# Performance work log

Hardware: AMD Instinct MI355X
Metric: run time of the kernel (lower is better)

## Reference

```python
import jax, jax.numpy as jnp
import numpy as np
import math

B, N, DIM = 2, 4096, 1024
H, D, M = 16, 64, 256


def setup_inputs() -> dict:
    key = jax.random.key(0)
    ks = jax.random.split(key, 6)
    s = 1.0 / math.sqrt(DIM)
    return {
        "x": jax.random.normal(ks[0], (B, N, DIM), dtype=jnp.float32),
        "w_q": jax.random.normal(ks[1], (DIM, H * D), dtype=jnp.float32) * s,
        "w_k": jax.random.normal(ks[2], (DIM, H * D), dtype=jnp.float32) * s,
        "w_v": jax.random.normal(ks[3], (DIM, H * D), dtype=jnp.float32) * s,
        "w_o": jax.random.normal(ks[4], (H * D, DIM), dtype=jnp.float32) * s,
        "b_o": jnp.zeros((DIM,), dtype=jnp.float32),
        "omega": jax.random.normal(ks[5], (M, D), dtype=jnp.float32),
    }


def _heads(t):
    # [B, N, H*D] -> [B, H, N, D]
    return t.reshape(B, N, H, D).transpose(0, 2, 1, 3)


def _phi(t, omega):
    # t: [B,H,N,D], omega: [M,D] -> [B,H,N,M]
    proj = jnp.einsum("bhnd,md->bhnm", t, omega)
    norm = 0.5 * jnp.sum(t * t, axis=-1, keepdims=True)
    return jnp.exp(proj - norm) / math.sqrt(M)


def reference(x, w_q, w_k, w_v, w_o, b_o, omega):
    q = _heads(x @ w_q)
    k = _heads(x @ w_k)
    v = _heads(x @ w_v)
    phi_q = _phi(q, omega)          # [B,H,N,M]
    phi_k = _phi(k, omega)          # [B,H,N,M]
    kv = jnp.einsum("bhnm,bhnd->bhmd", phi_k, v)   # [B,H,M,D]
    k_sum = phi_k.sum(axis=2)                       # [B,H,M]
    z = 1.0 / (jnp.einsum("bhnm,bhm->bhn", phi_q, k_sum) + 1e-6)
    out = jnp.einsum("bhnm,bhmd->bhnd", phi_q, kv) * z[..., None]
    out = out.transpose(0, 2, 1, 3).reshape(B, N, H * D)
    return out @ w_o + b_o
```

## Files before the change

kernel.cpp:

```cpp
#include <hip/hip_runtime.h>

#define DEVI __device__ __forceinline__

using f32x4 = __attribute__((ext_vector_type(4))) float;
using fvec4 = __attribute__((ext_vector_type(4))) float;
using s16x4 = __attribute__((ext_vector_type(4))) short;
using s16x8 = __attribute__((ext_vector_type(8))) short;

DEVI unsigned short f2bf_rn(float f) {
  union { float f; unsigned u; } v; v.f = f;
  unsigned r = v.u + 0x7fffu + ((v.u >> 16) & 1u);
  return (unsigned short)(r >> 16);
}
DEVI float bf2f(unsigned short h) {
  union { unsigned u; float f; } v; v.u = ((unsigned)h) << 16;
  return v.f;
}
DEVI f32x4 mfma16(s16x8 a, s16x8 b, f32x4 c) {
  return __builtin_amdgcn_mfma_f32_16x16x32_bf16(a, b, c, 0, 0, 0);
}
DEVI void gld16(const void* g, void* lds) {
  __builtin_amdgcn_global_load_lds(
      (const __attribute__((address_space(1))) unsigned int*)g,
      (__attribute__((address_space(3))) unsigned int*)lds, 16, 0, 0);
}

__global__ __launch_bounds__(256) void k_prep_all(
    const float* __restrict__ wq, const float* __restrict__ wk,
    const float* __restrict__ wv, const float* __restrict__ wo,
    const float* __restrict__ omega, const float* __restrict__ X,
    unsigned short* __restrict__ WTh, unsigned short* __restrict__ WOT,
    unsigned short* __restrict__ OMB,
    unsigned short* __restrict__ XH, unsigned short* __restrict__ XL)
{
  __shared__ float tile[64][65];
  const int z = blockIdx.z;
  const int t = threadIdx.x;
  if (z >= 5) {
    int s = z - 5;
    int bid = blockIdx.x * 16 + blockIdx.y;
    size_t i = (((size_t)s * 256 + bid) * 256 + t) * 8;
    fvec4 a = *(const fvec4*)&X[i];
    fvec4 b = *(const fvec4*)&X[i + 4];
    s16x8 hv, lv;
#pragma unroll
    for (int j = 0; j < 4; ++j) {
      unsigned short h = f2bf_rn(a[j]);
      hv[j] = (short)h; lv[j] = (short)f2bf_rn(a[j] - bf2f(h));
    }
#pragma unroll
    for (int j = 0; j < 4; ++j) {
      unsigned short h = f2bf_rn(b[j]);
      hv[4 + j] = (short)h; lv[4 + j] = (short)f2bf_rn(b[j] - bf2f(h));
    }
    *(s16x8*)&XH[i] = hv;
    *(s16x8*)&XL[i] = lv;
    return;
  }
  if (z == 4) {
    int bid = blockIdx.x * 16 + blockIdx.y;
    if (bid < 16) {
      int i = (bid * 256 + t) * 4;
      fvec4 v = *(const fvec4*)&omega[i];
      s16x4 hv;
#pragma unroll
      for (int q = 0; q < 4; ++q) hv[q] = (short)f2bf_rn(v[q]);
      *(s16x4*)&OMB[i] = hv;
    }
    return;
  }
  const float* src = (z == 0) ? wq : (z == 1) ? wk : (z == 2) ? wv : wo;
  const int k0 = blockIdx.x * 64;
  const int n0 = blockIdx.y * 64;
#pragma unroll
  for (int j = 0; j < 4; ++j) {
    int r = (t >> 4) + 16 * j;
    int c = (t & 15) * 4;
    fvec4 v = *(const fvec4*)&src[(size_t)(k0 + r) * 1024 + n0 + c];
#pragma unroll
    for (int i = 0; i < 4; ++i) tile[r][c + i] = v[i];
  }
  __syncthreads();
#pragma unroll
  for (int j = 0; j < 4; ++j) {
    int n = (t >> 4) + 16 * j;
    int kc = (t & 15) * 4;
    s16x4 hv;
#pragma unroll
    for (int i = 0; i < 4; ++i) hv[i] = (short)f2bf_rn(tile[kc + i][n]);
    if (z < 3) {
      *(s16x4*)&WTh[(size_t)(z * 1024 + n0 + n) * 1024 + k0 + kc] = hv;
    } else {
      *(s16x4*)&WOT[(size_t)(n0 + n) * 1024 + k0 + kc] = hv;
    }
  }
}

__global__ __launch_bounds__(256) void k_gemm_qkv(
    const unsigned short* __restrict__ XH, const unsigned short* __restrict__ XL,
    const unsigned short* __restrict__ WTh,
    unsigned short* __restrict__ QH, unsigned short* __restrict__ QL,
    unsigned short* __restrict__ KH, unsigned short* __restrict__ KL,
    unsigned short* __restrict__ VB)
{
  __shared__ unsigned short AH[2][128 * 32];
  __shared__ unsigned short BHs[2][128 * 32];
  __shared__ unsigned short AL[2][128 * 32];
  const int flat = blockIdx.y * 24 + blockIdx.x;
  const int swz = (flat & 7) * 192 + (flat >> 3);
  const int cb = swz % 24;
  const int rb = swz / 24;
  const int t = threadIdx.x;
  const int w = t >> 6, l = t & 63;
  const bool tp = (cb < 16);
  f32x4 acc[4][4];
#pragma unroll
  for (int a = 0; a < 4; ++a)
#pragma unroll
    for (int b = 0; b < 4; ++b) acc[a][b] = (f32x4)0.f;

  const int r0 = w * 32;
  const int lrow = l >> 2;
  const int lcol = (l & 3) * 8;
  const size_t gA = (size_t)(rb * 128 + r0 + lrow) * 1024 + lcol;
  const size_t gB = (size_t)(cb * 128 + r0 + lrow) * 1024 + lcol;
  const int lds0 = r0 * 32;
  const int lds1 = (r0 + 16) * 32;

  const int wm = (w & 1) * 64, wn = (w >> 1) * 64;
  const int lr = l & 15, ko = (l >> 4) * 8;

  auto STAGE = [&](int buf, int k0) {
    gld16(&XH[gA + k0], &AH[buf][lds0]);
    gld16(&XH[gA + (size_t)16 * 1024 + k0], &AH[buf][lds1]);
    if (tp) {
      gld16(&XL[gA + k0], &AL[buf][lds0]);
      gld16(&XL[gA + (size_t)16 * 1024 + k0], &AL[buf][lds1]);
    }
    gld16(&WTh[gB + k0], &BHs[buf][lds0]);
    gld16(&WTh[gB + (size_t)16 * 1024 + k0], &BHs[buf][lds1]);
  };

  STAGE(0, 0);
  int cur = 0;
  for (int ks = 0; ks < 32; ++ks) {
    if (ks < 31) {
      STAGE(cur ^ 1, (ks + 1) * 32);
      if (tp) asm volatile("s_waitcnt vmcnt(6)" ::: "memory");
      else    asm volatile("s_waitcnt vmcnt(4)" ::: "memory");
    } else {
      asm volatile("s_waitcnt vmcnt(0)" ::: "memory");
    }
    __builtin_amdgcn_s_barrier();
    asm volatile("" ::: "memory");
    s16x8 ah[4], al[4], bh[4];
#pragma unroll
    for (int f = 0; f < 4; ++f) {
      ah[f] = *(const s16x8*)&AH[cur][(wm + f * 16 + lr) * 32 + ko];
      bh[f] = *(const s16x8*)&BHs[cur][(wn + f * 16 + lr) * 32 + ko];
    }
    if (tp) {
#pragma unroll
      for (int f = 0; f < 4; ++f) al[f] = *(const s16x8*)&AL[cur][(wm + f * 16 + lr) * 32 + ko];
    }
#pragma unroll
    for (int fa = 0; fa < 4; ++fa)
#pragma unroll
      for (int fb = 0; fb < 4; ++fb) {
        acc[fa][fb] = mfma16(ah[fa], bh[fb], acc[fa][fb]);
        if (tp) acc[fa][fb] = mfma16(al[fa], bh[fb], acc[fa][fb]);
      }
    asm volatile("s_waitcnt lgkmcnt(0)" ::: "memory");
    __builtin_amdgcn_s_barrier();
    asm volatile("" ::: "memory");
    cur ^= 1;
  }
  const int lg = l >> 4;
#pragma unroll
  for (int fa = 0; fa < 4; ++fa)
#pragma unroll
    for (int r = 0; r < 4; ++r) {
      int row = rb * 128 + wm + fa * 16 + lg * 4 + r;
#pragma unroll
      for (int fb = 0; fb < 4; ++fb) {
        int col = cb * 128 + wn + fb * 16 + lr;
        float v = acc[fa][fb][r];
        if (tp) {
          unsigned short hs = f2bf_rn(v);
          unsigned short ls = f2bf_rn(v - bf2f(hs));
          if (cb < 8) {
            QH[(size_t)row * 1024 + col] = hs;
            QL[(size_t)row * 1024 + col] = ls;
          } else {
            KH[(size_t)row * 1024 + col - 1024] = hs;
            KL[(size_t)row * 1024 + col - 1024] = ls;
          }
        } else {
          VB[(size_t)row * 1024 + col - 2048] = f2bf_rn(v);
        }
      }
    }
}

__global__ __launch_bounds__(512, 1) void k_phik_kv(
    const unsigned short* __restrict__ KH, const unsigned short* __restrict__ KL,
    const unsigned short* __restrict__ VB,
    const unsigned short* __restrict__ OMB, float* __restrict__ KVP)
{
  __shared__ unsigned short KHs[64][72], KLs[64][72];
  __shared__ unsigned short PKT[128][72];
  __shared__ unsigned short AVT[80][72];
  __shared__ float norm_s[64];
  const int nc = blockIdx.x;
  const int bh = blockIdx.y;
  const int mh = blockIdx.z;
  const int b = bh >> 4, h = bh & 15;
  const int t = threadIdx.x, w = t >> 6, l = t & 63;
  const int lr = l & 15, lg = l >> 4, ko8 = lg * 8;
  const int mg = mh * 128 + w * 16 + lr;

  s16x8 omf[2];
#pragma unroll
  for (int ksub = 0; ksub < 2; ++ksub)
    omf[ksub] = *(const s16x8*)&OMB[(size_t)mg * 64 + ksub * 32 + ko8];

  for (int e = t; e < 16 * 64; e += 512) {
    int rr = e >> 6, cc = e & 63;
    AVT[64 + rr][cc] = (rr == 0) ? (unsigned short)0x3F80 : (unsigned short)0;
  }

  f32x4 acc2[5];
#pragma unroll
  for (int a = 0; a < 5; ++a) acc2[a] = (f32x4)0.f;

  for (int st = 0; st < 8; ++st) {
    const int n0 = nc * 512 + st * 64;
    __syncthreads();
    {
      int r = t >> 3, c8 = (t & 7) * 8;
      size_t o = (size_t)(b * 4096 + n0 + r) * 1024 + h * 64 + c8;
      s16x8 vh = *(const s16x8*)&KH[o];
      s16x8 vl = *(const s16x8*)&KL[o];
      *(s16x8*)&KHs[r][c8] = vh;
      *(s16x8*)&KLs[r][c8] = vl;
      float ss = 0.f;
#pragma unroll
      for (int i = 0; i < 8; ++i) {
        float q = bf2f((unsigned short)vh[i]) + bf2f((unsigned short)vl[i]);
        ss += q * q;
      }
      ss += __shfl_xor(ss, 1);
      ss += __shfl_xor(ss, 2);
      ss += __shfl_xor(ss, 4);
      if ((t & 7) == 0) norm_s[r] = 0.5f * ss;
    }
    {
      int n = t >> 3, dq = (t & 7) * 8;
      s16x8 v = *(const s16x8*)&VB[(size_t)(b * 4096 + n0 + n) * 1024 + h * 64 + dq];
#pragma unroll
      for (int i = 0; i < 8; ++i) AVT[dq + i][n] = (unsigned short)v[i];
    }
    __syncthreads();
    f32x4 acc[4];
#pragma unroll
    for (int a = 0; a < 4; ++a) acc[a] = (f32x4)0.f;
#pragma unroll
    for (int ksub = 0; ksub < 2; ++ksub) {
      int ko = ksub * 32 + ko8;
      s16x8 ah[4], al[4];
#pragma unroll
      for (int f = 0; f < 4; ++f) {
        ah[f] = *(const s16x8*)&KHs[f * 16 + lr][ko];
        al[f] = *(const s16x8*)&KLs[f * 16 + lr][ko];
      }
#pragma unroll
      for (int fa = 0; fa < 4; ++fa) {
        acc[fa] = mfma16(ah[fa], omf[ksub], acc[fa]);
        acc[fa] = mfma16(al[fa], omf[ksub], acc[fa]);
      }
    }
#pragma unroll
    for (int fa = 0; fa < 4; ++fa)
#pragma unroll
      for (int r = 0; r < 4; ++r) {
        int n = fa * 16 + lg * 4 + r;
        float nm = norm_s[n];
        int ml = w * 16 + lr;
        float p = __expf(acc[fa][r] - nm) * 0.0625f;
        PKT[ml][n] = f2bf_rn(p);
      }
    __syncthreads();
#pragma unroll
    for (int ksub = 0; ksub < 2; ++ksub) {
      int ko = ksub * 32 + ko8;
      s16x8 fA[5];
#pragma unroll
      for (int f = 0; f < 5; ++f) fA[f] = *(const s16x8*)&AVT[f * 16 + lr][ko];
      s16x8 fB = *(const s16x8*)&PKT[w * 16 + lr][ko];
#pragma unroll
      for (int fa = 0; fa < 5; ++fa) acc2[fa] = mfma16(fA[fa], fB, acc2[fa]);
    }
  }
#pragma unroll
  for (int fa = 0; fa < 5; ++fa)
#pragma unroll
    for (int r = 0; r < 4; ++r) {
      int dp = fa * 16 + lg * 4 + r;
      int m = mh * 128 + w * 16 + lr;
      KVP[(size_t)((bh * 8 + nc) * 80 + dp) * 256 + m] = acc2[fa][r];
    }
}

__global__ __launch_bounds__(256) void k_kv_reduce(
    const float* __restrict__ KVP, unsigned short* __restrict__ KVTB)
{
  int idx = blockIdx.x * 256 + threadIdx.x;
  if (idx >= 32 * 80 * 256) return;
  int bh = idx / (80 * 256);
  int rem = idx % (80 * 256);
  float s = 0.f;
#pragma unroll
  for (int nci = 0; nci < 8; ++nci) s += KVP[(size_t)(bh * 8 + nci) * 80 * 256 + rem];
  KVTB[idx] = f2bf_rn(s);
}

__global__ __launch_bounds__(256) void k_phiq_attn(
    const unsigned short* QH, const unsigned short* QL,
    const unsigned short* __restrict__ OMB,
    const unsigned short* __restrict__ KVTB,
    unsigned short* ATT)
{
  __shared__ unsigned short QHs[64][72], QLs[64][72];
  __shared__ unsigned short PQ[64][264];
  __shared__ float norm_s[64];
  const int nt = blockIdx.x;
  const int bh = blockIdx.y;
  const int t = threadIdx.x, w = t >> 6, l = t & 63;
  const int b = bh >> 4, h = bh & 15;
  const int lr = l & 15, lg = l >> 4, ko8 = lg * 8;

  s16x8 omf[2][4];
#pragma unroll
  for (int ksub = 0; ksub < 2; ++ksub)
#pragma unroll
    for (int f = 0; f < 4; ++f)
      omf[ksub][f] = *(const s16x8*)&OMB[(w * 64 + f * 16 + lr) * 64 + ksub * 32 + ko8];

  {
    int r = t >> 2, cq = (t & 3) * 4;
    float ss = 0.f;
#pragma unroll
    for (int j = 0; j < 4; ++j) {
      int c = cq + 16 * j;
      size_t o = (size_t)(b * 4096 + nt * 64 + r) * 1024 + h * 64 + c;
      s16x4 vh = *(const s16x4*)&QH[o];
      s16x4 vl = *(const s16x4*)&QL[o];
      *(s16x4*)&QHs[r][c] = vh;
      *(s16x4*)&QLs[r][c] = vl;
#pragma unroll
      for (int i = 0; i < 4; ++i) {
        float q = bf2f((unsigned short)vh[i]) + bf2f((unsigned short)vl[i]);
        ss += q * q;
      }
    }
    ss += __shfl_xor(ss, 1);
    ss += __shfl_xor(ss, 2);
    if ((t & 3) == 0) norm_s[r] = 0.5f * ss;
  }
  __syncthreads();
  f32x4 acc[4][4];
#pragma unroll
  for (int a = 0; a < 4; ++a)
#pragma unroll
    for (int bb = 0; bb < 4; ++bb) acc[a][bb] = (f32x4)0.f;
#pragma unroll
  for (int ksub = 0; ksub < 2; ++ksub) {
    int ko = ksub * 32 + ko8;
    s16x8 ah[4], al[4];
#pragma unroll
    for (int f = 0; f < 4; ++f) {
      ah[f] = *(const s16x8*)&QHs[f * 16 + lr][ko];
      al[f] = *(const s16x8*)&QLs[f * 16 + lr][ko];
    }
#pragma unroll
    for (int fa = 0; fa < 4; ++fa)
#pragma unroll
      for (int fb = 0; fb < 4; ++fb) {
        acc[fa][fb] = mfma16(ah[fa], omf[ksub][fb], acc[fa][fb]);
        acc[fa][fb] = mfma16(al[fa], omf[ksub][fb], acc[fa][fb]);
      }
  }
#pragma unroll
  for (int fa = 0; fa < 4; ++fa)
#pragma unroll
    for (int r = 0; r < 4; ++r) {
      int n = fa * 16 + lg * 4 + r;
      float nm = norm_s[n];
#pragma unroll
      for (int fb = 0; fb < 4; ++fb) {
        int m = w * 64 + fb * 16 + lr;
        float p = __expf(acc[fa][fb][r] - nm) * 0.0625f;
        PQ[n][m] = f2bf_rn(p);
      }
    }
  __syncthreads();
  const size_t kvbase = (size_t)bh * 80 * 256;
  f32x4 acc2[5];
#pragma unroll
  for (int bb = 0; bb < 5; ++bb) acc2[bb] = (f32x4)0.f;
  for (int ks = 0; ks < 8; ++ks) {
    const int m0 = ks * 32;
    s16x8 fA = *(const s16x8*)&PQ[w * 16 + lr][m0 + ko8];
    s16x8 fB[5];
#pragma unroll
    for (int f = 0; f < 5; ++f)
      fB[f] = *(const s16x8*)&KVTB[kvbase + (size_t)(f * 16 + lr) * 256 + m0 + ko8];
#pragma unroll
    for (int fb = 0; fb < 5; ++fb) acc2[fb] = mfma16(fA, fB[fb], acc2[fb]);
  }
#pragma unroll
  for (int r = 0; r < 4; ++r) {
    float den = __shfl(acc2[4][r], (l & 48));
    float z = 1.f / (den + 1e-6f);
    int n = nt * 64 + w * 16 + lg * 4 + r;
#pragma unroll
    for (int fb = 0; fb < 4; ++fb) {
      int col = h * 64 + fb * 16 + lr;
      ATT[(size_t)(b * 4096 + n) * 1024 + col] = f2bf_rn(acc2[fb][r] * z);
    }
  }
}

__global__ __launch_bounds__(256) void k_gemm_out(
    const unsigned short* __restrict__ ATT,
    const unsigned short* __restrict__ WOT,
    const float* __restrict__ b_o,
    float* __restrict__ OUT)
{
  __shared__ unsigned short As[3][128 * 32], Bs[3][128 * 32];
  const int flat = blockIdx.y * 8 + blockIdx.x;
  const int swz = (flat & 7) * 64 + (flat >> 3);
  const int cb = swz % 8;
  const int rb = swz / 8;
  const int t = threadIdx.x, w = t >> 6, l = t & 63;
  f32x4 acc[4][4];
#pragma unroll
  for (int a = 0; a < 4; ++a)
#pragma unroll
    for (int bb = 0; bb < 4; ++bb) acc[a][bb] = (f32x4)0.f;

  const int r0 = w * 32;
  const int lrow = l >> 2;
  const int lcol = (l & 3) * 8;
  const size_t gA = (size_t)(rb * 128 + r0 + lrow) * 1024 + lcol;
  const size_t gB = (size_t)(cb * 128 + r0 + lrow) * 1024 + lcol;
  const int lds0 = r0 * 32;
  const int lds1 = (r0 + 16) * 32;

  const int wm = (w & 1) * 64, wn = (w >> 1) * 64;
  const int lr = l & 15, ko = (l >> 4) * 8;

  auto STAGE = [&](int buf, int k0) {
    gld16(&ATT[gA + k0], &As[buf][lds0]);
    gld16(&ATT[gA + (size_t)16 * 1024 + k0], &As[buf][lds1]);
    gld16(&WOT[gB + k0], &Bs[buf][lds0]);
    gld16(&WOT[gB + (size_t)16 * 1024 + k0], &Bs[buf][lds1]);
  };

  STAGE(0, 0);
  STAGE(1, 32);
  int cur = 0;
  for (int ks = 0; ks < 32; ++ks) {
    if (ks < 30) {
      int nxt = (cur >= 1) ? cur - 1 : 2;
      STAGE(nxt, (ks + 2) * 32);
      asm volatile("s_waitcnt vmcnt(8)" ::: "memory");
    } else if (ks == 30) {
      asm volatile("s_waitcnt vmcnt(4)" ::: "memory");
    } else {
      asm volatile("s_waitcnt vmcnt(0)" ::: "memory");
    }
    __builtin_amdgcn_s_barrier();
    asm volatile("" ::: "memory");
    s16x8 fA[4], fB[4];
#pragma unroll
    for (int f = 0; f < 4; ++f) {
      fA[f] = *(const s16x8*)&As[cur][(wm + f * 16 + lr) * 32 + ko];
      fB[f] = *(const s16x8*)&Bs[cur][(wn + f * 16 + lr) * 32 + ko];
    }
#pragma unroll
    for (int fa = 0; fa < 4; ++fa)
#pragma unroll
      for (int fb = 0; fb < 4; ++fb) acc[fa][fb] = mfma16(fA[fa], fB[fb], acc[fa][fb]);
    asm volatile("s_waitcnt lgkmcnt(0)" ::: "memory");
    __builtin_amdgcn_s_barrier();
    asm volatile("" ::: "memory");
    cur = (cur < 2) ? cur + 1 : 0;
  }
  const int lg = l >> 4;
#pragma unroll
  for (int fa = 0; fa < 4; ++fa)
#pragma unroll
    for (int r = 0; r < 4; ++r) {
      int row = rb * 128 + wm + fa * 16 + lg * 4 + r;
#pragma unroll
      for (int fb = 0; fb < 4; ++fb) {
        int col = cb * 128 + wn + fb * 16 + lr;
        OUT[(size_t)row * 1024 + col] = acc[fa][fb][r] + b_o[col];
      }
    }
}

extern "C" void kernel_launch(void* const* d_in, const int* in_sizes, int n_in,
                              void* d_out, int out_size, void* d_ws, size_t ws_size,
                              hipStream_t stream)
{
  const float* x  = (const float*)d_in[0];
  const float* wq = (const float*)d_in[1];
  const float* wk = (const float*)d_in[2];
  const float* wv = (const float*)d_in[3];
  const float* wo = (const float*)d_in[4];
  const float* bo = (const float*)d_in[5];
  const float* om = (const float*)d_in[6];
  float* out = (float*)d_out;

  const size_t PLANE = (size_t)8192 * 1024 * 2;
  char* ws = (char*)d_ws;
  unsigned short* WOT = (unsigned short*)(ws);
  char* segB = ws + 2097152;
  char* segC = segB + 2 * PLANE;
  char* segD = segC + 4 * PLANE;
  char* segE = segD + 26214400;

  unsigned short* QH  = (unsigned short*)segB;
  unsigned short* QL  = (unsigned short*)(segB + PLANE);
  unsigned short* ATT = (unsigned short*)segB;

  unsigned short* KH  = (unsigned short*)segC;
  unsigned short* KL  = (unsigned short*)(segC + PLANE);
  unsigned short* VB  = (unsigned short*)(segC + 2 * PLANE);
  unsigned short* XH  = (unsigned short*)(segC + 3 * PLANE);

  unsigned short* WTh = (unsigned short*)segD;
  unsigned short* XL  = (unsigned short*)(segD + 6291456);
  float* KVP = (float*)segD;
  unsigned short* KVTB = (unsigned short*)segE;
  unsigned short* OMB  = (unsigned short*)(segE + 1310720);

  k_prep_all<<<dim3(16, 16, 21), 256, 0, stream>>>(wq, wk, wv, wo, om, x,
                                                   WTh, WOT, OMB, XH, XL);
  k_gemm_qkv<<<dim3(24, 64), 256, 0, stream>>>(XH, XL, WTh, QH, QL, KH, KL, VB);
  k_phik_kv<<<dim3(8, 32, 2), 512, 0, stream>>>(KH, KL, VB, OMB, KVP);
  k_kv_reduce<<<dim3(2560), 256, 0, stream>>>(KVP, KVTB);
  k_phiq_attn<<<dim3(64, 32), 256, 0, stream>>>(QH, QL, OMB, KVTB, ATT);
  k_gemm_out<<<dim3(8, 64), 256, 0, stream>>>(ATT, WOT, bo, out);
}
```

Baseline: 227.1 us.

## Pre-pack weights and KV into MFMA fragment order, load B directly to registers

The prep kernel now writes the QKV and output-projection weights in a fragment-packed layout matching the MFMA B-operand lane order. The two GEMMs then load B fragments straight from global memory into registers with one coalesced 16-byte load per lane, dropping the B LDS staging buffers. k_gemm_out also goes from triple to double buffering for A. KV reduce writes KV in the same packed layout so the attention kernel reads B fragments contiguously, and s_setprio is raised around the MFMA blocks. This cuts LDS traffic and footprint, but the global B loads now sit on the critical path with only the vmcnt wait hiding their latency.

```diff
diff --git a/kernel.cpp b/kernel.cpp
--- a/kernel.cpp
+++ b/kernel.cpp
@@ -25,11 +25,12 @@
       (__attribute__((address_space(3))) unsigned int*)lds, 16, 0, 0);
 }
 
+
 __global__ __launch_bounds__(256) void k_prep_all(
     const float* __restrict__ wq, const float* __restrict__ wk,
     const float* __restrict__ wv, const float* __restrict__ wo,
     const float* __restrict__ omega, const float* __restrict__ X,
-    unsigned short* __restrict__ WTh, unsigned short* __restrict__ WOT,
+    unsigned short* __restrict__ WFP, unsigned short* __restrict__ WOFP,
     unsigned short* __restrict__ OMB,
     unsigned short* __restrict__ XH, unsigned short* __restrict__ XL)
 {
@@ -88,23 +89,29 @@
     s16x4 hv;
 #pragma unroll
     for (int i = 0; i < 4; ++i) hv[i] = (short)f2bf_rn(tile[kc + i][n]);
+    const int kk = k0 + kc;
     if (z < 3) {
-      *(s16x4*)&WTh[(size_t)(z * 1024 + n0 + n) * 1024 + k0 + kc] = hv;
+      int ng = z * 1024 + n0 + n;
+      size_t o = ((size_t)((ng >> 4) * 32 + (kk >> 5)) * 512) +
+                 (size_t)(((ng & 15) | (((kk >> 3) & 3) << 4)) * 8) + (kk & 7);
+      *(s16x4*)&WFP[o] = hv;
     } else {
-      *(s16x4*)&WOT[(size_t)(n0 + n) * 1024 + k0 + kc] = hv;
+      int ng = n0 + n;
+      size_t o = ((size_t)((ng >> 4) * 32 + (kk >> 5)) * 512) +
+                 (size_t)(((ng & 15) | (((kk >> 3) & 3) << 4)) * 8) + (kk & 7);
+      *(s16x4*)&WOFP[o] = hv;
     }
   }
 }
 
 __global__ __launch_bounds__(256) void k_gemm_qkv(
     const unsigned short* __restrict__ XH, const unsigned short* __restrict__ XL,
-    const unsigned short* __restrict__ WTh,
+    const unsigned short* __restrict__ WFP,
     unsigned short* __restrict__ QH, unsigned short* __restrict__ QL,
     unsigned short* __restrict__ KH, unsigned short* __restrict__ KL,
     unsigned short* __restrict__ VB)
 {
   __shared__ unsigned short AH[2][128 * 32];
-  __shared__ unsigned short BHs[2][128 * 32];
   __shared__ unsigned short AL[2][128 * 32];
   const int flat = blockIdx.y * 24 + blockIdx.x;
   const int swz = (flat & 7) * 192 + (flat >> 3);
@@ -123,12 +130,16 @@
   const int lrow = l >> 2;
   const int lcol = (l & 3) * 8;
   const size_t gA = (size_t)(rb * 128 + r0 + lrow) * 1024 + lcol;
-  const size_t gB = (size_t)(cb * 128 + r0 + lrow) * 1024 + lcol;
   const int lds0 = r0 * 32;
   const int lds1 = (r0 + 16) * 32;
 
   const int wm = (w & 1) * 64, wn = (w >> 1) * 64;
   const int lr = l & 15, ko = (l >> 4) * 8;
+
+  const unsigned short* Bf[4];
+#pragma unroll
+  for (int f = 0; f < 4; ++f)
+    Bf[f] = &WFP[(size_t)(cb * 8 + (wn >> 4) + f) * 32 * 512 + l * 8];
 
   auto STAGE = [&](int buf, int k0) {
     gld16(&XH[gA + k0], &AH[buf][lds0]);
@@ -137,32 +148,32 @@
       gld16(&XL[gA + k0], &AL[buf][lds0]);
       gld16(&XL[gA + (size_t)16 * 1024 + k0], &AL[buf][lds1]);
     }
-    gld16(&WTh[gB + k0], &BHs[buf][lds0]);
-    gld16(&WTh[gB + (size_t)16 * 1024 + k0], &BHs[buf][lds1]);
   };
 
   STAGE(0, 0);
   int cur = 0;
   for (int ks = 0; ks < 32; ++ks) {
+    s16x8 bh[4];
+#pragma unroll
+    for (int f = 0; f < 4; ++f) bh[f] = *(const s16x8*)(Bf[f] + ks * 512);
+    asm volatile("" ::: "memory");
     if (ks < 31) {
       STAGE(cur ^ 1, (ks + 1) * 32);
-      if (tp) asm volatile("s_waitcnt vmcnt(6)" ::: "memory");
-      else    asm volatile("s_waitcnt vmcnt(4)" ::: "memory");
+      if (tp) asm volatile("s_waitcnt vmcnt(8)" ::: "memory");
+      else    asm volatile("s_waitcnt vmcnt(6)" ::: "memory");
     } else {
-      asm volatile("s_waitcnt vmcnt(0)" ::: "memory");
+      asm volatile("s_waitcnt vmcnt(4)" ::: "memory");
     }
     __builtin_amdgcn_s_barrier();
     asm volatile("" ::: "memory");
-    s16x8 ah[4], al[4], bh[4];
-#pragma unroll
-    for (int f = 0; f < 4; ++f) {
-      ah[f] = *(const s16x8*)&AH[cur][(wm + f * 16 + lr) * 32 + ko];
-      bh[f] = *(const s16x8*)&BHs[cur][(wn + f * 16 + lr) * 32 + ko];
-    }
+    s16x8 ah[4], al[4];
+#pragma unroll
+    for (int f = 0; f < 4; ++f) ah[f] = *(const s16x8*)&AH[cur][(wm + f * 16 + lr) * 32 + ko];
     if (tp) {
 #pragma unroll
       for (int f = 0; f < 4; ++f) al[f] = *(const s16x8*)&AL[cur][(wm + f * 16 + lr) * 32 + ko];
     }
+    __builtin_amdgcn_s_setprio(1);
 #pragma unroll
     for (int fa = 0; fa < 4; ++fa)
 #pragma unroll
@@ -170,6 +181,7 @@
         acc[fa][fb] = mfma16(ah[fa], bh[fb], acc[fa][fb]);
         if (tp) acc[fa][fb] = mfma16(al[fa], bh[fb], acc[fa][fb]);
       }
+    __builtin_amdgcn_s_setprio(0);
     asm volatile("s_waitcnt lgkmcnt(0)" ::: "memory");
     __builtin_amdgcn_s_barrier();
     asm volatile("" ::: "memory");
@@ -312,22 +324,25 @@
 }
 
 __global__ __launch_bounds__(256) void k_kv_reduce(
-    const float* __restrict__ KVP, unsigned short* __restrict__ KVTB)
+    const float* __restrict__ KVP, unsigned short* __restrict__ KVFB)
 {
   int idx = blockIdx.x * 256 + threadIdx.x;
   if (idx >= 32 * 80 * 256) return;
   int bh = idx / (80 * 256);
   int rem = idx % (80 * 256);
+  int dp = rem >> 8, m = rem & 255;
   float s = 0.f;
 #pragma unroll
   for (int nci = 0; nci < 8; ++nci) s += KVP[(size_t)(bh * 8 + nci) * 80 * 256 + rem];
-  KVTB[idx] = f2bf_rn(s);
+  int kc = m >> 5, f = dp >> 4;
+  int lane = (dp & 15) | (((m >> 3) & 3) << 4);
+  KVFB[(((size_t)bh * 8 + kc) * 5 + f) * 512 + lane * 8 + (m & 7)] = f2bf_rn(s);
 }
 
 __global__ __launch_bounds__(256) void k_phiq_attn(
     const unsigned short* QH, const unsigned short* QL,
     const unsigned short* __restrict__ OMB,
-    const unsigned short* __restrict__ KVTB,
+    const unsigned short* __restrict__ KVFB,
     unsigned short* ATT)
 {
   __shared__ unsigned short QHs[64][72], QLs[64][72];
@@ -404,7 +419,6 @@
       }
     }
   __syncthreads();
-  const size_t kvbase = (size_t)bh * 80 * 256;
   f32x4 acc2[5];
 #pragma unroll
   for (int bb = 0; bb < 5; ++bb) acc2[bb] = (f32x4)0.f;
@@ -414,7 +428,7 @@
     s16x8 fB[5];
 #pragma unroll
     for (int f = 0; f < 5; ++f)
-      fB[f] = *(const s16x8*)&KVTB[kvbase + (size_t)(f * 16 + lr) * 256 + m0 + ko8];
+      fB[f] = *(const s16x8*)&KVFB[(((size_t)bh * 8 + ks) * 5 + f) * 512 + l * 8];
 #pragma unroll
     for (int fb = 0; fb < 5; ++fb) acc2[fb] = mfma16(fA, fB[fb], acc2[fb]);
   }
@@ -433,11 +447,11 @@
 
 __global__ __launch_bounds__(256) void k_gemm_out(
     const unsigned short* __restrict__ ATT,
-    const unsigned short* __restrict__ WOT,
+    const unsigned short* __restrict__ WOFP,
     const float* __restrict__ b_o,
     float* __restrict__ OUT)
 {
-  __shared__ unsigned short As[3][128 * 32], Bs[3][128 * 32];
+  __shared__ unsigned short As[2][128 * 32];
   const int flat = blockIdx.y * 8 + blockIdx.x;
   const int swz = (flat & 7) * 64 + (flat >> 3);
   const int cb = swz % 8;
@@ -453,49 +467,50 @@
   const int lrow = l >> 2;
   const int lcol = (l & 3) * 8;
   const size_t gA = (size_t)(rb * 128 + r0 + lrow) * 1024 + lcol;
-  const size_t gB = (size_t)(cb * 128 + r0 + lrow) * 1024 + lcol;
   const int lds0 = r0 * 32;
   const int lds1 = (r0 + 16) * 32;
 
   const int wm = (w & 1) * 64, wn = (w >> 1) * 64;
   const int lr = l & 15, ko = (l >> 4) * 8;
+
+  const unsigned short* Bf[4];
+#pragma unroll
+  for (int f = 0; f < 4; ++f)
+    Bf[f] = &WOFP[(size_t)(cb * 8 + (wn >> 4) + f) * 32 * 512 + l * 8];
 
   auto STAGE = [&](int buf, int k0) {
     gld16(&ATT[gA + k0], &As[buf][lds0]);
     gld16(&ATT[gA + (size_t)16 * 1024 + k0], &As[buf][lds1]);
-    gld16(&WOT[gB + k0], &Bs[buf][lds0]);
-    gld16(&WOT[gB + (size_t)16 * 1024 + k0], &Bs[buf][lds1]);
   };
 
   STAGE(0, 0);
-  STAGE(1, 32);
   int cur = 0;
   for (int ks = 0; ks < 32; ++ks) {
-    if (ks < 30) {
-      int nxt = (cur >= 1) ? cur - 1 : 2;
-      STAGE(nxt, (ks + 2) * 32);
-      asm volatile("s_waitcnt vmcnt(8)" ::: "memory");
-    } else if (ks == 30) {
+    s16x8 fB[4];
+#pragma unroll
+    for (int f = 0; f < 4; ++f) fB[f] = *(const s16x8*)(Bf[f] + ks * 512);
+    asm volatile("" ::: "memory");
+    if (ks < 31) {
+      STAGE(cur ^ 1, (ks + 1) * 32);
+      asm volatile("s_waitcnt vmcnt(6)" ::: "memory");
+    } else {
       asm volatile("s_waitcnt vmcnt(4)" ::: "memory");
-    } else {
-      asm volatile("s_waitcnt vmcnt(0)" ::: "memory");
     }
     __builtin_amdgcn_s_barrier();
     asm volatile("" ::: "memory");
-    s16x8 fA[4], fB[4];
-#pragma unroll
-    for (int f = 0; f < 4; ++f) {
-      fA[f] = *(const s16x8*)&As[cur][(wm + f * 16 + lr) * 32 + ko];
-      fB[f] = *(const s16x8*)&Bs[cur][(wn + f * 16 + lr) * 32 + ko];
-    }
+    s16x8 fA[4];
+#pragma unroll
+    for (int f = 0; f < 4; ++f) fA[f] = *(const s16x8*)&As[cur][(wm + f * 16 + lr) * 32 + ko];
+    __builtin_amdgcn_s_setprio(1);
 #pragma unroll
     for (int fa = 0; fa < 4; ++fa)
 #pragma unroll
       for (int fb = 0; fb < 4; ++fb) acc[fa][fb] = mfma16(fA[fa], fB[fb], acc[fa][fb]);
+    __builtin_amdgcn_s_setprio(0);
     asm volatile("s_waitcnt lgkmcnt(0)" ::: "memory");
     __builtin_amdgcn_s_barrier();
     asm volatile("" ::: "memory");
-    cur = (cur < 2) ? cur + 1 : 0;
+    cur ^= 1;
   }
   const int lg = l >> 4;
 #pragma unroll
@@ -526,7 +541,7 @@
 
   const size_t PLANE = (size_t)8192 * 1024 * 2;
   char* ws = (char*)d_ws;
-  unsigned short* WOT = (unsigned short*)(ws);
+  unsigned short* WOFP = (unsigned short*)(ws);
   char* segB = ws + 2097152;
   char* segC = segB + 2 * PLANE;
   char* segD = segC + 4 * PLANE;
@@ -541,17 +556,17 @@
   unsigned short* VB  = (unsigned short*)(segC + 2 * PLANE);
   unsigned short* XH  = (unsigned short*)(segC + 3 * PLANE);
 
-  unsigned short* WTh = (unsigned short*)segD;
+  unsigned short* WFP = (unsigned short*)segD;
   unsigned short* XL  = (unsigned short*)(segD + 6291456);
   float* KVP = (float*)segD;
-  unsigned short* KVTB = (unsigned short*)segE;
+  unsigned short* KVFB = (unsigned short*)segE;
   unsigned short* OMB  = (unsigned short*)(segE + 1310720);
 
   k_prep_all<<<dim3(16, 16, 21), 256, 0, stream>>>(wq, wk, wv, wo, om, x,
-                                                   WTh, WOT, OMB, XH, XL);
-  k_gemm_qkv<<<dim3(24, 64), 256, 0, stream>>>(XH, XL, WTh, QH, QL, KH, KL, VB);
+                                                   WFP, WOFP, OMB, XH, XL);
+  k_gemm_qkv<<<dim3(24, 64), 256, 0, stream>>>(XH, XL, WFP, QH, QL, KH, KL, VB);
   k_phik_kv<<<dim3(8, 32, 2), 512, 0, stream>>>(KH, KL, VB, OMB, KVP);
-  k_kv_reduce<<<dim3(2560), 256, 0, stream>>>(KVP, KVTB);
-  k_phiq_attn<<<dim3(64, 32), 256, 0, stream>>>(QH, QL, OMB, KVTB, ATT);
-  k_gemm_out<<<dim3(8, 64), 256, 0, stream>>>(ATT, WOT, bo, out);
-}
+  k_kv_reduce<<<dim3(2560), 256, 0, stream>>>(KVP, KVFB);
+  k_phiq_attn<<<dim3(64, 32), 256, 0, stream>>>(QH, QL, OMB, KVFB, ATT);
+  k_gemm_out<<<dim3(8, 64), 256, 0, stream>>>(ATT, WOFP, bo, out);
+}
```

After: 210.8 us, median of 3. 7.2% less time.
